# Kernel optimization log

Hardware: AMD Instinct MI355X
Metric: run time of the kernel (lower is better)

## Reference

```python
import jax, jax.numpy as jnp
import numpy as np

DIM = 512
HEADS = 8
DH = DIM // HEADS          # 64
M = DIM // 2               # 256 landmarks
PINV_ITERS = 6
KERNEL = 33                # residual_conv_kernel (lucidrains default)
SCALE = DH ** -0.5
LN_EPS = 1e-5


def setup_inputs() -> dict:
    key = jax.random.key(0)
    ks = jax.random.split(key, 6)
    b, n = 4, 4096
    x = jax.random.normal(ks[0], (b, n, DIM), jnp.float32)
    ln_w = jnp.ones((DIM,), jnp.float32)
    ln_b = jnp.zeros((DIM,), jnp.float32)
    w_qkv = jax.random.normal(ks[1], (DIM, 3 * DIM), jnp.float32) / np.float32(np.sqrt(DIM))
    w_out = jax.random.normal(ks[2], (DIM, DIM), jnp.float32) / np.float32(np.sqrt(DIM))
    b_out = jnp.zeros((DIM,), jnp.float32)
    # depthwise Conv2d(heads, heads, (33,1), groups=heads, bias=False): OIHW = (8,1,33,1)
    conv_w = jax.random.normal(ks[3], (HEADS, 1, KERNEL, 1), jnp.float32) / np.float32(np.sqrt(KERNEL))
    # admin_torch.as_module(8): residual x*omega + f(x), omega learnable scalar init sqrt(8)
    omega = jnp.asarray(np.sqrt(8.0), jnp.float32)
    return dict(x=x, ln_w=ln_w, ln_b=ln_b, w_qkv=w_qkv, w_out=w_out,
                b_out=b_out, conv_w=conv_w, omega=omega)


def _layernorm(x, w, b):
    mu = x.mean(-1, keepdims=True)
    var = x.var(-1, keepdims=True)
    return (x - mu) * jax.lax.rsqrt(var + LN_EPS) * w + b


def _moore_penrose_pinv(x, iters):
    # Newton-Schulz iteration, exactly as lucidrains nystrom-attention
    abs_x = jnp.abs(x)
    col = abs_x.sum(-1)
    row = abs_x.sum(-2)
    z = jnp.swapaxes(x, -1, -2) / (jnp.max(col) * jnp.max(row))
    I = jnp.eye(x.shape[-1], dtype=x.dtype)
    for _ in range(iters):
        xz = x @ z
        z = 0.25 * z @ (13. * I - xz @ (15. * I - xz @ (7. * I - xz)))
    return z


def reference(x, ln_w, ln_b, w_qkv, w_out, b_out, conv_w, omega):
    b, n, _ = x.shape
    nx = _layernorm(x, ln_w, ln_b)
    qkv = nx @ w_qkv                                # [b, n, 3*dim]
    q, k, v = jnp.split(qkv, 3, axis=-1)
    to_heads = lambda t: t.reshape(b, n, HEADS, DH).transpose(0, 2, 1, 3)  # bhnd
    q = to_heads(q) * SCALE
    k = to_heads(k)
    v = to_heads(v)
    l = n // M                                      # tokens per landmark group
    q_l = q.reshape(b, HEADS, M, l, DH).mean(3)     # [b,h,m,d]
    k_l = k.reshape(b, HEADS, M, l, DH).mean(3)
    sim1 = jnp.einsum('bhid,bhjd->bhij', q, k_l)    # [b,h,n,m]
    sim2 = jnp.einsum('bhid,bhjd->bhij', q_l, k_l)  # [b,h,m,m]
    sim3 = jnp.einsum('bhid,bhjd->bhij', q_l, k)    # [b,h,m,n]
    a1 = jax.nn.softmax(sim1, -1)
    a2 = jax.nn.softmax(sim2, -1)
    a3 = jax.nn.softmax(sim3, -1)
    a2_inv = _moore_penrose_pinv(a2, PINV_ITERS)
    out = (a1 @ a2_inv) @ (a3 @ v)                  # [b,h,n,d]
    # residual depthwise conv along the sequence dim of v
    res = jax.lax.conv_general_dilated(
        v, conv_w, window_strides=(1, 1),
        padding=((KERNEL // 2, KERNEL // 2), (0, 0)),
        dimension_numbers=('NCHW', 'OIHW', 'NCHW'),
        feature_group_count=HEADS)
    out = out + res
    out = out.transpose(0, 2, 1, 3).reshape(b, n, HEADS * DH)
    out = out @ w_out + b_out                       # to_out (dropout is eval no-op)
    return x * omega + out                          # admin residual
```

## Files before the change

### kernel.cpp

```cpp
#include <hip/hip_runtime.h>
#include <math.h>

#define B_    4
#define N_    4096
#define DIM_  512
#define H_    8
#define DH_   64
#define M_    256
#define LGRP  16
#define BH_   (B_*H_)
#define SCALE_ 0.125f
#define LN_EPS_ 1e-5f

#define SZ_QKVH (B_*H_*N_*DH_)
#define SZ_LM   (BH_*M_*DH_)
#define SZ_MM   (BH_*M_*M_)

typedef unsigned short ushort_t;
typedef __attribute__((ext_vector_type(8))) short bfrag8;
typedef __attribute__((ext_vector_type(4))) float fvec4;

__device__ __forceinline__ ushort_t f2b(float f) {
    unsigned u = __float_as_uint(f);
    unsigned r = (u + 0x7fffu + ((u >> 16) & 1u)) >> 16;
    return (ushort_t)r;
}
__device__ __forceinline__ float b2f(ushort_t s) {
    return __uint_as_float(((unsigned)s) << 16);
}

__device__ __forceinline__ void gload16(const ushort_t* g, ushort_t* l) {
    __builtin_amdgcn_global_load_lds(
        (const __attribute__((address_space(1))) void*)g,
        (__attribute__((address_space(3))) void*)l, 16, 0, 0);
}

__global__ __launch_bounds__(256) void ln_kernel(const float* __restrict__ x,
                                                 const float* __restrict__ w,
                                                 const float* __restrict__ bb,
                                                 ushort_t* __restrict__ nxb) {
    int row = blockIdx.x;
    int t = threadIdx.x;
    const float* xr = x + (size_t)row * DIM_;
    float v0 = xr[t], v1 = xr[t + 256];
    float s = v0 + v1, sq = v0 * v0 + v1 * v1;
    __shared__ float ls[4], lq[4];
    for (int off = 32; off > 0; off >>= 1) {
        s  += __shfl_down(s, off);
        sq += __shfl_down(sq, off);
    }
    int wid = t >> 6, lid = t & 63;
    if (lid == 0) { ls[wid] = s; lq[wid] = sq; }
    __syncthreads();
    if (t == 0) {
        float S = 0, Q = 0;
        for (int i = 0; i < 4; i++) { S += ls[i]; Q += lq[i]; }
        ls[0] = S; lq[0] = Q;
    }
    __syncthreads();
    float mean = ls[0] * (1.f / DIM_);
    float var  = lq[0] * (1.f / DIM_) - mean * mean;
    float rs = rsqrtf(var + LN_EPS_);
    ushort_t* o = nxb + (size_t)row * DIM_;
    o[t]       = f2b((v0 - mean) * rs * w[t]       + bb[t]);
    o[t + 256] = f2b((v1 - mean) * rs * w[t + 256] + bb[t + 256]);
}

__global__ __launch_bounds__(256) void tcast(const float* __restrict__ in,
                                             ushort_t* __restrict__ outT,
                                             int R, int C) {
    __shared__ float tile[32][33];
    int c0 = blockIdx.x * 32, r0 = blockIdx.y * 32;
    int t = threadIdx.x;
    #pragma unroll
    for (int u = 0; u < 4; u++) {
        int lin = t + 256 * u;
        int r = lin >> 5, c = lin & 31;
        tile[r][c] = in[(size_t)(r0 + r) * C + c0 + c];
    }
    __syncthreads();
    #pragma unroll
    for (int u = 0; u < 4; u++) {
        int lin = t + 256 * u;
        int cc = lin >> 5, rr = lin & 31;
        outT[(size_t)(c0 + cc) * R + r0 + rr] = f2b(tile[rr][cc]);
    }
}

template<int EPI>
__global__ __launch_bounds__(256) void gemm_bt128(const ushort_t* __restrict__ A,
                                                  const ushort_t* __restrict__ BT,
                                                  ushort_t* __restrict__ qb,
                                                  ushort_t* __restrict__ kb,
                                                  ushort_t* __restrict__ vb,
                                                  const float* __restrict__ x,
                                                  const float* __restrict__ bo,
                                                  const float* __restrict__ omega,
                                                  float* __restrict__ out) {
    const int K = 512;
    __shared__ __align__(16) ushort_t smem[4 * 128 * 64];
    int t = threadIdx.x;
    int lin = blockIdx.x + blockIdx.y * gridDim.x;
    int nwg = gridDim.x * gridDim.y;
    int wg  = (lin & 7) * (nwg >> 3) + (lin >> 3);
    int n0 = (wg % gridDim.x) * 128, m0 = (wg / gridDim.x) * 128;
    int w = t >> 6, lane = t & 63;
    int wr = (w >> 1) * 64, wc = (w & 1) * 64;
    int l15 = lane & 15, quad = lane >> 4, kq = quad * 8;
    int lrow = lane >> 3, lc8 = (lane & 7) * 8;
    int scol = lc8 ^ ((lrow & 7) << 3);
    int sw   = (l15 & 7) << 3;
    fvec4 acc[4][4] = {};

    auto stage = [&](int buf, int kc) {
        ushort_t* Ad = smem + buf * 16384;
        ushort_t* Bd = Ad + 8192;
        #pragma unroll
        for (int u = 0; u < 4; u++) {
            int r0 = (w << 5) + (u << 3);
            int row = r0 + lrow;
            const ushort_t* ga;
            if (EPI == 0) {
                ga = A + (size_t)(m0 + row) * K + kc + scol;
            } else {
                int grow = m0 + row; int b_ = grow >> 12, nn = grow & 4095;
                ga = A + (((size_t)(b_ * H_ + (kc >> 6)) * N_ + nn) << 6) + scol;
            }
            gload16(ga, Ad + r0 * 64);
            gload16(BT + (size_t)(n0 + row) * K + kc + scol, Bd + r0 * 64);
        }
    };

    stage(0, 0);
    __syncthreads();
    int cur = 0;
    for (int kt = 0; kt < 8; ++kt) {
        if (kt < 7) stage(cur ^ 1, (kt + 1) * 64);
        const ushort_t* As = smem + cur * 16384;
        const ushort_t* Bs = As + 8192;
        #pragma unroll
        for (int ks = 0; ks < 64; ks += 32) {
            int kcol = (ks + kq) ^ sw;
            bfrag8 a[4], b[4];
            #pragma unroll
            for (int r = 0; r < 4; r++) a[r] = *(bfrag8*)(As + (wr + r * 16 + l15) * 64 + kcol);
            #pragma unroll
            for (int c = 0; c < 4; c++) b[c] = *(bfrag8*)(Bs + (wc + c * 16 + l15) * 64 + kcol);
            #pragma unroll
            for (int r = 0; r < 4; r++)
                #pragma unroll
                for (int c = 0; c < 4; c++)
                    acc[r][c] = __builtin_amdgcn_mfma_f32_16x16x32_bf16(a[r], b[c], acc[r][c], 0, 0, 0);
        }
        __syncthreads();
        cur ^= 1;
    }

    if (EPI == 0) {
        int sec = n0 >> 9;
        float mul = (sec == 0) ? SCALE_ : 1.0f;
        ushort_t (*Ct)[132] = (ushort_t(*)[132])smem;
        #pragma unroll
        for (int r = 0; r < 4; r++) {
            #pragma unroll
            for (int reg = 0; reg < 4; reg++) {
                int lr = wr + r * 16 + quad * 4 + reg;
                #pragma unroll
                for (int c = 0; c < 4; c++) {
                    int lc = wc + c * 16 + l15;
                    Ct[lr][lc] = f2b(acc[r][c][reg] * mul);
                }
            }
        }
        __syncthreads();
        int row = t & 127, half = t >> 7;
        int grow = m0 + row; int b_ = grow >> 12, nn = grow & 4095;
        int head = ((n0 & 511) >> 6) + half;
        ushort_t* dstbuf = (sec == 0) ? qb : ((sec == 1) ? kb : vb);
        ushort_t* dp = dstbuf + (((size_t)(b_ * H_ + head) * N_ + nn) << 6);
        #pragma unroll
        for (int i = 0; i < 8; i++)
            *(uint4*)(dp + i * 8) = *(uint4*)&Ct[row][half * 64 + i * 8];
    } else {
        float om = omega[0];
        #pragma unroll
        for (int r = 0; r < 4; r++) {
            #pragma unroll
            for (int reg = 0; reg < 4; reg++) {
                int grow = m0 + wr + r * 16 + quad * 4 + reg;
                #pragma unroll
                for (int c = 0; c < 4; c++) {
                    int gcol = n0 + wc + c * 16 + l15;
                    size_t o = (size_t)grow * DIM_ + gcol;
                    out[o] = om * x[o] + bo[gcol] + acc[r][c][reg];
                }
            }
        }
    }
}

__global__ __launch_bounds__(256) void landmark_kernel(const ushort_t* __restrict__ q,
                                                       const ushort_t* __restrict__ k,
                                                       ushort_t* __restrict__ ql,
                                                       ushort_t* __restrict__ kl) {
    int idx = blockIdx.x * 256 + threadIdx.x;
    const ushort_t* src = blockIdx.y ? k : q;
    ushort_t* dst = blockIdx.y ? kl : ql;
    int d8 = (idx & 7) * 8;
    int m = (idx >> 3) & 255;
    int bh = idx >> 11;
    const ushort_t* p = src + (((size_t)bh * N_) + m * LGRP) * DH_ + d8;
    float s[8] = {};
    #pragma unroll
    for (int j = 0; j < LGRP; j++) {
        union { uint4 u4; ushort_t sv[8]; } val;
        val.u4 = *(const uint4*)(p + (size_t)j * DH_);
        #pragma unroll
        for (int e = 0; e < 8; e++) s[e] += b2f(val.sv[e]);
    }
    union { uint4 u4; ushort_t sv[8]; } o;
    #pragma unroll
    for (int e = 0; e < 8; e++) o.sv[e] = f2b(s[e] * (1.f / LGRP));
    *(uint4*)(dst + ((size_t)bh * M_ + m) * DH_ + d8) = o.u4;
}

__global__ __launch_bounds__(256) void sim2_softmax(const ushort_t* __restrict__ ql,
                                                    const ushort_t* __restrict__ kl,
                                                    float* __restrict__ a2,
                                                    ushort_t* __restrict__ a2b) {
    int i = blockIdx.x, bh = blockIdx.y, j = threadIdx.x;
    __shared__ float qrow[64];
    __shared__ float red[256];
    if (j < 64) qrow[j] = b2f(ql[((size_t)bh * M_ + i) * DH_ + j]);
    __syncthreads();
    const ushort_t* kr = kl + ((size_t)bh * M_ + j) * DH_;
    float s = 0;
    #pragma unroll
    for (int d = 0; d < 64; d++) s += qrow[d] * b2f(kr[d]);
    red[j] = s; __syncthreads();
    for (int off = 128; off > 0; off >>= 1) {
        if (j < off) red[j] = fmaxf(red[j], red[j + off]);
        __syncthreads();
    }
    float mx = red[0]; __syncthreads();
    float p = __expf(s - mx);
    red[j] = p; __syncthreads();
    for (int off = 128; off > 0; off >>= 1) {
        if (j < off) red[j] += red[j + off];
        __syncthreads();
    }
    float res = p / red[0];
    size_t o = ((size_t)bh * M_ + i) * M_ + j;
    a2[o] = res;
    a2b[o] = f2b(res);
}

__global__ void zero2(unsigned* p) { if (threadIdx.x < 2) p[threadIdx.x] = 0u; }

__global__ __launch_bounds__(256) void colpart(const float* __restrict__ a2,
                                               float* __restrict__ cs2) {
    int bh = blockIdx.x, s = blockIdx.y, t = threadIdx.x;
    const float* A = a2 + ((size_t)bh << 16) + (size_t)s * 32 * M_;
    float cs = 0.f;
    #pragma unroll
    for (int i = 0; i < 32; i++) cs += A[(size_t)i * M_ + t];
    cs2[((size_t)s * BH_ + bh) * M_ + t] = cs;
}

__global__ __launch_bounds__(256) void colmax(const float* __restrict__ cs2, unsigned* red) {
    int bh = blockIdx.x, t = threadIdx.x;
    float v = 0.f;
    #pragma unroll
    for (int s = 0; s < 8; s++) v += cs2[((size_t)s * BH_ + bh) * M_ + t];
    __shared__ float lr[256];
    lr[t] = v; __syncthreads();
    for (int off = 128; off > 0; off >>= 1) {
        if (t < off) lr[t] = fmaxf(lr[t], lr[t + off]);
        __syncthreads();
    }
    if (t == 0) atomicMax(red, __float_as_uint(lr[0]));
}

__global__ __launch_bounds__(256) void pinv_init2(const float* __restrict__ a2,
                                                  const unsigned* __restrict__ red,
                                                  ushort_t* __restrict__ zA,
                                                  ushort_t* __restrict__ zAT) {
    __shared__ float tile[32][33];
    int bt = blockIdx.z; int j0 = blockIdx.x * 32, i0 = blockIdx.y * 32;
    float invd = 1.f / __uint_as_float(red[0]);
    const float* Ab = a2 + ((size_t)bt << 16);
    size_t bo = (size_t)bt << 16;
    int t = threadIdx.x;
    #pragma unroll
    for (int u = 0; u < 4; u++) {
        int lin = t + 256 * u; int r = lin >> 5, c = lin & 31;
        float vv = Ab[(size_t)(i0 + r) * M_ + j0 + c] * invd;
        tile[r][c] = vv;
        zAT[bo + (size_t)(i0 + r) * M_ + j0 + c] = f2b(vv);
    }
    __syncthreads();
    #pragma unroll
    for (int u = 0; u < 4; u++) {
        int lin = t + 256 * u; int cc = lin >> 5, rr = lin & 31;
        zA[bo + (size_t)(j0 + cc) * M_ + i0 + rr] = f2b(tile[rr][cc]);
    }
}

__global__ __launch_bounds__(256) void gemm_pinv(const ushort_t* __restrict__ A,
                                                 const ushort_t* __restrict__ BT,
                                                 ushort_t* __restrict__ outN,
                                                 ushort_t* __restrict__ outT,
                                                 ushort_t* __restrict__ outT1,
                                                 float* __restrict__ outF,
                                                 float coefI, float scale) {
    __shared__ __align__(16) ushort_t smem[2 * 8192];
    int t = threadIdx.x;
    int lin = blockIdx.x + (blockIdx.y << 2) + (blockIdx.z << 4);
    int wg  = (lin & 7) * 64 + (lin >> 3);
    int n0 = (wg & 3) * 64, m0 = ((wg >> 2) & 3) * 64;
    int bt = wg >> 4;
    const ushort_t* Ab = A + ((size_t)bt << 16);
    const ushort_t* Bb = BT + ((size_t)bt << 16);
    int w = t >> 6, lane = t & 63;
    int wr = (w >> 1) * 32, wc = (w & 1) * 32;
    int l15 = lane & 15, quad = lane >> 4, kq = quad * 8;
    int lrow = lane >> 3, lc8 = (lane & 7) * 8;
    int scol = lc8 ^ ((lrow & 7) << 3);
    int sw   = (l15 & 7) << 3;
    fvec4 acc[2][2] = {};

    auto stage = [&](int buf, int kc) {
        ushort_t* Ad = smem + buf * 8192;
        ushort_t* Bd = Ad + 4096;
        #pragma unroll
        for (int u = 0; u < 2; u++) {
            int r0 = (w << 4) + (u << 3);
            int row = r0 + lrow;
            gload16(Ab + (size_t)(m0 + row) * M_ + kc + scol, Ad + r0 * 64);
            gload16(Bb + (size_t)(n0 + row) * M_ + kc + scol, Bd + r0 * 64);
        }
    };

    stage(0, 0);
    __syncthreads();
    int cur = 0;
    for (int kt = 0; kt < 4; ++kt) {
        if (kt < 3) stage(cur ^ 1, (kt + 1) * 64);
        const ushort_t* As = smem + cur * 8192;
        const ushort_t* Bs = As + 4096;
        #pragma unroll
        for (int ks = 0; ks < 64; ks += 32) {
            int kcol = (ks + kq) ^ sw;
            bfrag8 a[2], b[2];
            #pragma unroll
            for (int r = 0; r < 2; r++) a[r] = *(bfrag8*)(As + (wr + r * 16 + l15) * 64 + kcol);
            #pragma unroll
            for (int c = 0; c < 2; c++) b[c] = *(bfrag8*)(Bs + (wc + c * 16 + l15) * 64 + kcol);
            #pragma unroll
            for (int r = 0; r < 2; r++)
                #pragma unroll
                for (int c = 0; c < 2; c++)
                    acc[r][c] = __builtin_amdgcn_mfma_f32_16x16x32_bf16(a[r], b[c], acc[r][c], 0, 0, 0);
        }
        __syncthreads();
        cur ^= 1;
    }

    size_t bto = (size_t)bt << 16;
    if (outN || outF) {
        #pragma unroll
        for (int r = 0; r < 2; r++) {
            #pragma unroll
            for (int reg = 0; reg < 4; reg++) {
                int grow = m0 + wr + r * 16 + quad * 4 + reg;
                #pragma unroll
                for (int c = 0; c < 2; c++) {
                    int gcol = n0 + wc + c * 16 + l15;
                    float cv = scale * acc[r][c][reg] + (grow == gcol ? coefI : 0.f);
                    if (outN) outN[bto + (size_t)grow * M_ + gcol] = f2b(cv);
                    if (outF) outF[bto + (size_t)grow * M_ + gcol] = cv;
                }
            }
        }
    }
    if (outT || outT1) {
        ushort_t (*Ct)[65] = (ushort_t(*)[65])&smem[0];
        #pragma unroll
        for (int r = 0; r < 2; r++) {
            #pragma unroll
            for (int reg = 0; reg < 4; reg++) {
                int lr = wr + r * 16 + quad * 4 + reg;
                #pragma unroll
                for (int c = 0; c < 2; c++) {
                    int lc = wc + c * 16 + l15;
                    float cv = scale * acc[r][c][reg] + ((m0 + lr) == (n0 + lc) ? coefI : 0.f);
                    Ct[lr][lc] = f2b(cv);
                }
            }
        }
        __syncthreads();
        int j = t & 63, quarter = t >> 6, i0 = quarter * 16;
        #pragma unroll
        for (int vq = 0; vq < 2; vq++) {
            union { uint4 u4; ushort_t s[8]; } o1, o2;
            #pragma unroll
            for (int e = 0; e < 8; e++) {
                int il = i0 + vq * 8 + e;
                ushort_t bv = Ct[il][j];
                o1.s[e] = bv;
                o2.s[e] = f2b(((m0 + il) == (n0 + j) ? 7.f : 0.f) - b2f(bv));
            }
            size_t dst = bto + (size_t)(n0 + j) * M_ + m0 + i0 + vq * 8;
            if (outT)  *(uint4*)&outT[dst]  = o1.u4;
            if (outT1) *(uint4*)&outT1[dst] = o2.u4;
        }
    }
}

template<int NCH, int TRANSV>
__global__ __launch_bounds__(256) void flash_mfma(const ushort_t* __restrict__ Q,
                                                  const ushort_t* __restrict__ K,
                                                  const ushort_t* __restrict__ V,
                                                  ushort_t* __restrict__ Obf,
                                                  float* __restrict__ Opart,
                                                  float* __restrict__ lout,
                                                  int nq, int nk) {
    int bh = blockIdx.y;
    int nqt = nq >> 6;
    int qt = blockIdx.x % nqt;
    int ch = blockIdx.x / nqt;
    int q0 = qt * 64;
    int chunk = nk / NCH;
    int j0 = ch * chunk, j1 = j0 + chunk;

    __shared__ __align__(16) ushort_t qs[64][72];
    __shared__ __align__(16) ushort_t ks[64][72];
    __shared__ __align__(16) ushort_t vts[64][72];
    __shared__ __align__(16) ushort_t pb[64][72];

    int t = threadIdx.x;
    int w = t >> 6, lane = t & 63;
    int l15 = lane & 15, quad = lane >> 4, kq = quad * 8;
    int wrow = w * 16;

    const ushort_t* Qb = Q + ((size_t)bh * nq + q0) * DH_;
    #pragma unroll
    for (int u = 0; u < 2; u++) {
        int lin = t + 256 * u;
        int r = lin >> 3, cc = (lin & 7) * 8;
        *(uint4*)&qs[r][cc] = *(const uint4*)(Qb + r * DH_ + cc);
    }

    fvec4 Oacc[4];
    #pragma unroll
    for (int nt = 0; nt < 4; nt++)
        #pragma unroll
        for (int reg = 0; reg < 4; reg++) Oacc[nt][reg] = 0.f;
    float l_[4] = {0.f, 0.f, 0.f, 0.f};

    const ushort_t* VTbase = V + (size_t)bh * DH_ * nk;

    uint4 kreg[2], vreg[2];
    auto loadkv = [&](int j) {
        const ushort_t* Kb = K + ((size_t)bh * nk + j) * DH_;
        #pragma unroll
        for (int u = 0; u < 2; u++) {
            int lin = t + 256 * u;
            int r = lin >> 3, cc = (lin & 7) * 8;
            kreg[u] = *(const uint4*)(Kb + r * DH_ + cc);
            if (TRANSV == 0)
                vreg[u] = *(const uint4*)(VTbase + (size_t)r * nk + j + cc);
            else
                vreg[u] = *(const uint4*)(V + ((size_t)(bh * nk + j + r)) * DH_ + cc);
        }
    };
    auto writekv = [&]() {
        #pragma unroll
        for (int u = 0; u < 2; u++) {
            int lin = t + 256 * u;
            int r = lin >> 3, cc = (lin & 7) * 8;
            *(uint4*)&ks[r][cc] = kreg[u];
            if (TRANSV == 0) {
                *(uint4*)&vts[r][cc] = vreg[u];
            } else {
                union { uint4 u4; ushort_t s[8]; } vv;
                vv.u4 = vreg[u];
                #pragma unroll
                for (int m = 0; m < 8; m++) vts[cc + m][r] = vv.s[m];
            }
        }
    };

    loadkv(j0);
    for (int j = j0; j < j1; j += 64) {
        writekv();
        __syncthreads();
        if (j + 64 < j1) loadkv(j + 64);

        fvec4 S[4];
        #pragma unroll
        for (int ct = 0; ct < 4; ct++)
            #pragma unroll
            for (int reg = 0; reg < 4; reg++) S[ct][reg] = 0.f;
        bfrag8 aq0 = *(bfrag8*)&qs[wrow + l15][kq];
        bfrag8 aq1 = *(bfrag8*)&qs[wrow + l15][32 + kq];
        #pragma unroll
        for (int ct = 0; ct < 4; ct++) {
            bfrag8 b0 = *(bfrag8*)&ks[ct * 16 + l15][kq];
            bfrag8 b1 = *(bfrag8*)&ks[ct * 16 + l15][32 + kq];
            S[ct] = __builtin_amdgcn_mfma_f32_16x16x32_bf16(aq0, b0, S[ct], 0, 0, 0);
            S[ct] = __builtin_amdgcn_mfma_f32_16x16x32_bf16(aq1, b1, S[ct], 0, 0, 0);
        }

        float ps[4] = {0.f, 0.f, 0.f, 0.f};
        #pragma unroll
        for (int ct = 0; ct < 4; ct++) {
            #pragma unroll
            for (int reg = 0; reg < 4; reg++) {
                float pv = __expf(S[ct][reg]);
                ps[reg] += pv;
                pb[wrow + quad * 4 + reg][ct * 16 + l15] = f2b(pv);
            }
        }
        #pragma unroll
        for (int reg = 0; reg < 4; reg++) {
            float s = ps[reg];
            s += __shfl_xor(s, 1);
            s += __shfl_xor(s, 2);
            s += __shfl_xor(s, 4);
            s += __shfl_xor(s, 8);
            l_[reg] += s;
        }

        bfrag8 ap0 = *(bfrag8*)&pb[wrow + l15][kq];
        bfrag8 ap1 = *(bfrag8*)&pb[wrow + l15][32 + kq];
        #pragma unroll
        for (int nt = 0; nt < 4; nt++) {
            bfrag8 b0 = *(bfrag8*)&vts[nt * 16 + l15][kq];
            bfrag8 b1 = *(bfrag8*)&vts[nt * 16 + l15][32 + kq];
            Oacc[nt] = __builtin_amdgcn_mfma_f32_16x16x32_bf16(ap0, b0, Oacc[nt], 0, 0, 0);
            Oacc[nt] = __builtin_amdgcn_mfma_f32_16x16x32_bf16(ap1, b1, Oacc[nt], 0, 0, 0);
        }
        __syncthreads();
    }

    if (NCH == 1) {
        #pragma unroll
        for (int reg = 0; reg < 4; reg++) {
            float inv = 1.f / l_[reg];
            #pragma unroll
            for (int nt = 0; nt < 4; nt++)
                qs[wrow + quad * 4 + reg][nt * 16 + l15] = f2b(Oacc[nt][reg] * inv);
        }
        __syncthreads();
        ushort_t* Ob = Obf + ((size_t)bh * nq + q0) * DH_;
        #pragma unroll
        for (int u = 0; u < 2; u++) {
            int lin = t + 256 * u;
            int r = lin >> 3, i = (lin & 7) * 8;
            *(uint4*)(Ob + (size_t)r * DH_ + i) = *(uint4*)&qs[r][i];
        }
    } else {
        float (*Of)[68] = (float(*)[68])&ks[0][0];
        #pragma unroll
        for (int reg = 0; reg < 4; reg++)
            #pragma unroll
            for (int nt = 0; nt < 4; nt++)
                Of[wrow + quad * 4 + reg][nt * 16 + l15] = Oacc[nt][reg];
        size_t rows_per_ch = (size_t)BH_ * nq;
        size_t rowbase = (size_t)ch * rows_per_ch + (size_t)bh * nq + q0;
        if (l15 == 0) {
            #pragma unroll
            for (int reg = 0; reg < 4; reg++)
                lout[rowbase + wrow + quad * 4 + reg] = l_[reg];
        }
        __syncthreads();
        int orow = t >> 2, oc = (t & 3) * 16;
        float* Od = Opart + (rowbase + orow) * DH_ + oc;
        #pragma unroll
        for (int i = 0; i < 4; i++) {
            float4 v4 = make_float4(Of[orow][oc + i * 4], Of[orow][oc + i * 4 + 1],
                                    Of[orow][oc + i * 4 + 2], Of[orow][oc + i * 4 + 3]);
            *(float4*)(Od + i * 4) = v4;
        }
    }
}

__global__ __launch_bounds__(256) void flash_combine(const float* __restrict__ apart,
                                                     const float* __restrict__ lpart,
                                                     ushort_t* __restrict__ a3vb) {
    int idx = blockIdx.x * 256 + threadIdx.x;
    int d = idx & 63; int row = idx >> 6;
    const int R = BH_ * M_;
    size_t e = (size_t)row * DH_ + d;
    const size_t CH = (size_t)R * DH_;
    float l = 0.f, o = 0.f;
    #pragma unroll
    for (int s = 0; s < 4; s++) {
        l += lpart[row + (size_t)s * R];
        o += apart[e + (size_t)s * CH];
    }
    a3vb[e] = f2b(o / l);
}

__global__ __launch_bounds__(256) void flash_big(const ushort_t* __restrict__ Q,
                                                 const ushort_t* __restrict__ K,
                                                 const ushort_t* __restrict__ VT,
                                                 ushort_t* __restrict__ Obf) {
    const int nq = N_, nk = M_;
    int bh = blockIdx.y;
    int q0 = blockIdx.x * 256;
    __shared__ __align__(16) ushort_t ks[64][72];
    __shared__ __align__(16) ushort_t vts[64][72];
    __shared__ __align__(16) ushort_t pb[2][64][72];

    int t = threadIdx.x;
    int w = t >> 6, lane = t & 63;
    int l15 = lane & 15, quad = lane >> 4, kq = quad * 8;
    int wrow = w * 16;

    bfrag8 aq[4][2];
    const ushort_t* Qb = Q + ((size_t)bh * nq + q0) * DH_;
    #pragma unroll
    for (int s = 0; s < 4; s++) {
        #pragma unroll
        for (int u = 0; u < 2; u++) {
            int lin = t + 256 * u;
            int r = lin >> 3, cc = (lin & 7) * 8;
            *(uint4*)&pb[0][r][cc] = *(const uint4*)(Qb + (size_t)(s * 64 + r) * DH_ + cc);
        }
        __syncthreads();
        aq[s][0] = *(bfrag8*)&pb[0][wrow + l15][kq];
        aq[s][1] = *(bfrag8*)&pb[0][wrow + l15][32 + kq];
        __syncthreads();
    }

    fvec4 Oacc[4][4];
    #pragma unroll
    for (int s = 0; s < 4; s++)
        #pragma unroll
        for (int nt = 0; nt < 4; nt++)
            #pragma unroll
            for (int reg = 0; reg < 4; reg++) Oacc[s][nt][reg] = 0.f;
    float l_[4][4];
    #pragma unroll
    for (int s = 0; s < 4; s++)
        #pragma unroll
        for (int reg = 0; reg < 4; reg++) l_[s][reg] = 0.f;

    const ushort_t* VTb = VT + (size_t)bh * DH_ * nk;
    uint4 kreg[2], vreg[2];
    auto loadkv = [&](int j) {
        const ushort_t* Kb = K + ((size_t)bh * nk + j) * DH_;
        #pragma unroll
        for (int u = 0; u < 2; u++) {
            int lin = t + 256 * u;
            int r = lin >> 3, cc = (lin & 7) * 8;
            kreg[u] = *(const uint4*)(Kb + (size_t)r * DH_ + cc);
            vreg[u] = *(const uint4*)(VTb + (size_t)r * nk + j + cc);
        }
    };

    loadkv(0);
    for (int j = 0; j < nk; j += 64) {
        #pragma unroll
        for (int u = 0; u < 2; u++) {
            int lin = t + 256 * u;
            int r = lin >> 3, cc = (lin & 7) * 8;
            *(uint4*)&ks[r][cc] = kreg[u];
            *(uint4*)&vts[r][cc] = vreg[u];
        }
        __syncthreads();
        if (j + 64 < nk) loadkv(j + 64);

        #pragma unroll
        for (int s = 0; s < 4; s++) {
            fvec4 S[4];
            #pragma unroll
            for (int ct = 0; ct < 4; ct++)
                #pragma unroll
                for (int reg = 0; reg < 4; reg++) S[ct][reg] = 0.f;
            #pragma unroll
            for (int ct = 0; ct < 4; ct++) {
                bfrag8 b0 = *(bfrag8*)&ks[ct * 16 + l15][kq];
                bfrag8 b1 = *(bfrag8*)&ks[ct * 16 + l15][32 + kq];
                S[ct] = __builtin_amdgcn_mfma_f32_16x16x32_bf16(aq[s][0], b0, S[ct], 0, 0, 0);
                S[ct] = __builtin_amdgcn_mfma_f32_16x16x32_bf16(aq[s][1], b1, S[ct], 0, 0, 0);
            }
            float ps[4] = {0.f, 0.f, 0.f, 0.f};
            #pragma unroll
            for (int ct = 0; ct < 4; ct++) {
                #pragma unroll
                for (int reg = 0; reg < 4; reg++) {
                    float pv = __expf(S[ct][reg]);
                    ps[reg] += pv;
                    pb[s & 1][wrow + quad * 4 + reg][ct * 16 + l15] = f2b(pv);
                }
            }
            #pragma unroll
            for (int reg = 0; reg < 4; reg++) {
                float sm = ps[reg];
                sm += __shfl_xor(sm, 1);
                sm += __shfl_xor(sm, 2);
                sm += __shfl_xor(sm, 4);
                sm += __shfl_xor(sm, 8);
                l_[s][reg] += sm;
            }
            bfrag8 ap0 = *(bfrag8*)&pb[s & 1][wrow + l15][kq];
            bfrag8 ap1 = *(bfrag8*)&pb[s & 1][wrow + l15][32 + kq];
            #pragma unroll
            for (int nt = 0; nt < 4; nt++) {
                bfrag8 v0 = *(bfrag8*)&vts[nt * 16 + l15][kq];
                bfrag8 v1 = *(bfrag8*)&vts[nt * 16 + l15][32 + kq];
                Oacc[s][nt] = __builtin_amdgcn_mfma_f32_16x16x32_bf16(ap0, v0, Oacc[s][nt], 0, 0, 0);
                Oacc[s][nt] = __builtin_amdgcn_mfma_f32_16x16x32_bf16(ap1, v1, Oacc[s][nt], 0, 0, 0);
            }
        }
        __syncthreads();
    }

    ushort_t* Ob = Obf + ((size_t)bh * nq + q0) * DH_;
    #pragma unroll
    for (int s = 0; s < 4; s++) {
        #pragma unroll
        for (int reg = 0; reg < 4; reg++) {
            float inv = 1.f / l_[s][reg];
            #pragma unroll
            for (int nt = 0; nt < 4; nt++)
                pb[0][wrow + quad * 4 + reg][nt * 16 + l15] = f2b(Oacc[s][nt][reg] * inv);
        }
        __syncthreads();
        #pragma unroll
        for (int u = 0; u < 2; u++) {
            int lin = t + 256 * u;
            int r = lin >> 3, i = (lin & 7) * 8;
            *(uint4*)(Ob + (size_t)(s * 64 + r) * DH_ + i) = *(uint4*)&pb[0][r][i];
        }
        __syncthreads();
    }
}

__global__ __launch_bounds__(256) void wm_mfma(const ushort_t* __restrict__ Z,
                                               const ushort_t* __restrict__ A3V,
                                               ushort_t* __restrict__ WmT) {
    __shared__ __align__(16) ushort_t As[64][72];
    __shared__ __align__(16) ushort_t Bs[64][72];
    int bh = blockIdx.y;
    int i0 = blockIdx.x * 64;
    const ushort_t* Zb = Z + ((size_t)bh << 16);
    const ushort_t* Ab = A3V + ((size_t)bh << 14);
    int t = threadIdx.x;
    int w = t >> 6, lane = t & 63;
    int wr = (w >> 1) * 32, wc = (w & 1) * 32;
    int l15 = lane & 15, quad = lane >> 4, kq = quad * 8;
    fvec4 acc[2][2] = {};
    int rbase = t >> 3, c8 = (t & 7) * 8;

    for (int kc = 0; kc < M_; kc += 64) {
        #pragma unroll
        for (int u = 0; u < 2; u++) {
            int rr = rbase + 32 * u;
            *(float4*)&Bs[rr][c8] = *(const float4*)(Zb + (size_t)(i0 + rr) * M_ + kc + c8);
            union { uint4 u4; ushort_t s[8]; } av;
            av.u4 = *(const uint4*)(Ab + (size_t)(kc + rr) * DH_ + c8);
            #pragma unroll
            for (int m = 0; m < 8; m++) As[c8 + m][rr] = av.s[m];
        }
        __syncthreads();
        #pragma unroll
        for (int ks = 0; ks < 64; ks += 32) {
            bfrag8 a[2], b[2];
            #pragma unroll
            for (int r = 0; r < 2; r++) a[r] = *(bfrag8*)&As[wr + r * 16 + l15][ks + kq];
            #pragma unroll
            for (int c = 0; c < 2; c++) b[c] = *(bfrag8*)&Bs[wc + c * 16 + l15][ks + kq];
            #pragma unroll
            for (int r = 0; r < 2; r++)
                #pragma unroll
                for (int c = 0; c < 2; c++)
                    acc[r][c] = __builtin_amdgcn_mfma_f32_16x16x32_bf16(a[r], b[c], acc[r][c], 0, 0, 0);
        }
        __syncthreads();
    }
    #pragma unroll
    for (int r = 0; r < 2; r++) {
        #pragma unroll
        for (int reg = 0; reg < 4; reg++) {
            int drow = wr + r * 16 + quad * 4 + reg;
            ushort_t* dp = WmT + ((size_t)bh * DH_ + drow) * M_;
            #pragma unroll
            for (int c = 0; c < 2; c++)
                dp[i0 + wc + c * 16 + l15] = f2b(acc[r][c][reg]);
        }
    }
}

__global__ __launch_bounds__(256) void conv_kernel(const ushort_t* __restrict__ V,
                                                   const float* __restrict__ cw,
                                                   const ushort_t* __restrict__ ctxb,
                                                   ushort_t* __restrict__ outb) {
    int bh = blockIdx.y;
    int h = bh & 7;
    int i0 = blockIdx.x * 64;
    __shared__ float vb[96][64];
    __shared__ float wloc[33];
    int t = threadIdx.x;
    if (t < 33) wloc[t] = cw[h * 33 + t];
    #pragma unroll
    for (int u = 0; u < 3; u++) {
        int lin = t + 256 * u;
        int r = lin >> 3, cc = (lin & 7) * 8;
        int gi = i0 - 16 + r;
        union { uint4 u4; ushort_t s[8]; } val;
        if (gi >= 0 && gi < N_)
            val.u4 = *(const uint4*)(V + ((size_t)bh * N_ + gi) * DH_ + cc);
        else
            val.u4 = make_uint4(0, 0, 0, 0);
        #pragma unroll
        for (int m = 0; m < 8; m++) vb[r][cc + m] = b2f(val.s[m]);
    }
    __syncthreads();
    int d = t & 63, rb = t >> 6;
    for (int u = 0; u < 16; u++) {
        int r = rb * 16 + u;
        float s = 0.f;
        #pragma unroll
        for (int kk = 0; kk < 33; kk++) s += wloc[kk] * vb[r + kk][d];
        size_t o = ((size_t)bh * N_ + i0 + r) * DH_ + d;
        outb[o] = f2b(b2f(ctxb[o]) + s);
    }
}

extern "C" void kernel_launch(void* const* d_in, const int* in_sizes, int n_in,
                              void* d_out, int out_size, void* d_ws, size_t ws_size,
                              hipStream_t stream) {
    const float* x      = (const float*)d_in[0];
    const float* ln_w   = (const float*)d_in[1];
    const float* ln_b   = (const float*)d_in[2];
    const float* w_qkv  = (const float*)d_in[3];
    const float* w_out  = (const float*)d_in[4];
    const float* b_out  = (const float*)d_in[5];
    const float* conv_w = (const float*)d_in[6];
    const float* omega  = (const float*)d_in[7];
    float* out = (float*)d_out;

    float* fp = (float*)d_ws;
    float* a2    = fp;              fp += SZ_MM;
    float* apart = fp;              fp += SZ_QKVH / 4;
    float* lpart = fp;              fp += 4 * BH_ * M_;
    float* cs2   = fp;              fp += 8 * BH_ * M_;
    ushort_t* us = (ushort_t*)fp;
    ushort_t* wqkvT = us;           us += DIM_ * 3 * DIM_;
    ushort_t* woT   = us;           us += DIM_ * DIM_;
    ushort_t* a2b   = us;           us += SZ_MM;
    ushort_t* zA    = us;           us += SZ_MM;
    ushort_t* zAT   = us;           us += SZ_MM;
    ushort_t* zB    = us;           us += SZ_MM;
    ushort_t* zBT   = us;           us += SZ_MM;
    ushort_t* qb    = us;           us += SZ_QKVH;
    ushort_t* kb    = us;           us += SZ_QKVH;
    ushort_t* vb    = us;           us += SZ_QKVH;
    ushort_t* ctxb  = us;           us += SZ_QKVH;
    ushort_t* outhb = us;           us += SZ_QKVH;
    ushort_t* ql    = us;           us += SZ_LM;
    ushort_t* kl    = us;           us += SZ_LM;
    ushort_t* WmT   = us;           us += SZ_LM;
    ushort_t* a3vb  = us;           us += SZ_LM;
    unsigned* red   = (unsigned*)us;
    ushort_t* nxb = outhb;
    ushort_t* xz  = ctxb;
    ushort_t* t1T = xz  + SZ_MM;
    ushort_t* t2T = t1T + SZ_MM;
    ushort_t* t3T = t2T + SZ_MM;

    ln_kernel<<<B_ * N_, 256, 0, stream>>>(x, ln_w, ln_b, nxb);
    tcast<<<dim3(48, 16), 256, 0, stream>>>(w_qkv, wqkvT, DIM_, 3 * DIM_);
    tcast<<<dim3(16, 16), 256, 0, stream>>>(w_out, woT, DIM_, DIM_);
    gemm_bt128<0><<<dim3(12, 128), 256, 0, stream>>>(nxb, wqkvT, qb, kb, vb,
                                                     nullptr, nullptr, nullptr, nullptr);
    landmark_kernel<<<dim3(256, 2), 256, 0, stream>>>(qb, kb, ql, kl);
    sim2_softmax<<<dim3(M_, BH_), 256, 0, stream>>>(ql, kl, a2, a2b);
    zero2<<<1, 64, 0, stream>>>(red);
    colpart<<<dim3(BH_, 8), 256, 0, stream>>>(a2, cs2);
    colmax<<<BH_, 256, 0, stream>>>(cs2, red);
    pinv_init2<<<dim3(8, 8, 32), 256, 0, stream>>>(a2, red, zA, zAT);

    ushort_t* za = zA;  ushort_t* zaT = zAT;
    ushort_t* zb = zB;  ushort_t* zbT = zBT;
    for (int it = 0; it < 6; it++) {
        gemm_pinv<<<dim3(4, 4, BH_), 256, 0, stream>>>(a2b, zaT, xz, nullptr, t1T, nullptr, 0.f, 1.f);
        gemm_pinv<<<dim3(4, 4, BH_), 256, 0, stream>>>(xz, t1T, nullptr, t2T, nullptr, nullptr, 15.f, -1.f);
        gemm_pinv<<<dim3(4, 4, BH_), 256, 0, stream>>>(xz, t2T, nullptr, t3T, nullptr, nullptr, 13.f, -1.f);
        gemm_pinv<<<dim3(4, 4, BH_), 256, 0, stream>>>(za, t3T, zb, (it < 5) ? zbT : nullptr,
                                                       nullptr, nullptr, 0.f, 0.25f);
        ushort_t* tp;
        tp = za; za = zb; zb = tp;
        tp = zaT; zaT = zbT; zbT = tp;
    }

    flash_mfma<4, 1><<<dim3(16, BH_), 256, 0, stream>>>(ql, kb, vb, nullptr, apart, lpart, M_, N_);
    flash_combine<<<(BH_ * M_ * DH_) / 256, 256, 0, stream>>>(apart, lpart, a3vb);
    wm_mfma<<<dim3(4, BH_), 256, 0, stream>>>(za, a3vb, WmT);
    flash_big<<<dim3(N_ / 256, BH_), 256, 0, stream>>>(qb, kl, WmT, ctxb);
    conv_kernel<<<dim3(N_ / 64, BH_), 256, 0, stream>>>(vb, conv_w, ctxb, outhb);
    gemm_bt128<1><<<dim3(4, 128), 256, 0, stream>>>(outhb, woT, nullptr, nullptr, nullptr,
                                                    x, b_out, omega, out);
}
```

Baseline: 488.0 us.

## Process all 256 landmark queries per block in a3·v to reuse K/V tiles

```diff
diff --git a/kernel.cpp b/kernel.cpp
--- a/kernel.cpp
+++ b/kernel.cpp
@@ -417,166 +417,149 @@
     }
 }
 
-template<int NCH, int TRANSV>
-__global__ __launch_bounds__(256) void flash_mfma(const ushort_t* __restrict__ Q,
-                                                  const ushort_t* __restrict__ K,
-                                                  const ushort_t* __restrict__ V,
-                                                  ushort_t* __restrict__ Obf,
-                                                  float* __restrict__ Opart,
-                                                  float* __restrict__ lout,
-                                                  int nq, int nk) {
-    int bh = blockIdx.y;
-    int nqt = nq >> 6;
-    int qt = blockIdx.x % nqt;
-    int ch = blockIdx.x / nqt;
-    int q0 = qt * 64;
-    int chunk = nk / NCH;
-    int j0 = ch * chunk, j1 = j0 + chunk;
-
-    __shared__ __align__(16) ushort_t qs[64][72];
-    __shared__ __align__(16) ushort_t ks[64][72];
-    __shared__ __align__(16) ushort_t vts[64][72];
-    __shared__ __align__(16) ushort_t pb[64][72];
+__global__ __launch_bounds__(256) void flash_a3v(const ushort_t* __restrict__ Q,
+                                                 const ushort_t* __restrict__ K,
+                                                 const ushort_t* __restrict__ V,
+                                                 float* __restrict__ Opart,
+                                                 float* __restrict__ lout) {
+    const int nk = N_;
+    const int CHUNK = N_ / 8;
+    int bh = blockIdx.y, ch = blockIdx.x;
+    int j0 = ch * CHUNK, j1 = j0 + CHUNK;
+
+    __shared__ __align__(16) ushort_t smem[4 * 64 * 72];
+    ushort_t (*ks)[72]  = (ushort_t(*)[72])smem;
+    ushort_t (*vts)[72] = (ushort_t(*)[72])(smem + 64 * 72);
+    ushort_t (*pb)[64][72] = (ushort_t(*)[64][72])(smem + 2 * 64 * 72);
 
     int t = threadIdx.x;
     int w = t >> 6, lane = t & 63;
     int l15 = lane & 15, quad = lane >> 4, kq = quad * 8;
     int wrow = w * 16;
 
-    const ushort_t* Qb = Q + ((size_t)bh * nq + q0) * DH_;
-    #pragma unroll
-    for (int u = 0; u < 2; u++) {
-        int lin = t + 256 * u;
-        int r = lin >> 3, cc = (lin & 7) * 8;
-        *(uint4*)&qs[r][cc] = *(const uint4*)(Qb + r * DH_ + cc);
-    }
-
-    fvec4 Oacc[4];
-    #pragma unroll
-    for (int nt = 0; nt < 4; nt++)
-        #pragma unroll
-        for (int reg = 0; reg < 4; reg++) Oacc[nt][reg] = 0.f;
-    float l_[4] = {0.f, 0.f, 0.f, 0.f};
-
-    const ushort_t* VTbase = V + (size_t)bh * DH_ * nk;
+    bfrag8 aq[4][2];
+    const ushort_t* Qb = Q + (size_t)bh * M_ * DH_;
+    #pragma unroll
+    for (int s = 0; s < 4; s++) {
+        #pragma unroll
+        for (int u = 0; u < 2; u++) {
+            int lin = t + 256 * u;
+            int r = lin >> 3, cc = (lin & 7) * 8;
+            *(uint4*)&pb[0][r][cc] = *(const uint4*)(Qb + (size_t)(s * 64 + r) * DH_ + cc);
+        }
+        __syncthreads();
+        aq[s][0] = *(bfrag8*)&pb[0][wrow + l15][kq];
+        aq[s][1] = *(bfrag8*)&pb[0][wrow + l15][32 + kq];
+        __syncthreads();
+    }
+
+    fvec4 Oacc[4][4];
+    #pragma unroll
+    for (int s = 0; s < 4; s++)
+        #pragma unroll
+        for (int nt = 0; nt < 4; nt++)
+            #pragma unroll
+            for (int reg = 0; reg < 4; reg++) Oacc[s][nt][reg] = 0.f;
+    float l_[4][4];
+    #pragma unroll
+    for (int s = 0; s < 4; s++)
+        #pragma unroll
+        for (int reg = 0; reg < 4; reg++) l_[s][reg] = 0.f;
 
     uint4 kreg[2], vreg[2];
     auto loadkv = [&](int j) {
         const ushort_t* Kb = K + ((size_t)bh * nk + j) * DH_;
+        const ushort_t* Vb = V + ((size_t)bh * nk + j) * DH_;
         #pragma unroll
         for (int u = 0; u < 2; u++) {
             int lin = t + 256 * u;
             int r = lin >> 3, cc = (lin & 7) * 8;
-            kreg[u] = *(const uint4*)(Kb + r * DH_ + cc);
-            if (TRANSV == 0)
-                vreg[u] = *(const uint4*)(VTbase + (size_t)r * nk + j + cc);
-            else
-                vreg[u] = *(const uint4*)(V + ((size_t)(bh * nk + j + r)) * DH_ + cc);
+            kreg[u] = *(const uint4*)(Kb + (size_t)r * DH_ + cc);
+            vreg[u] = *(const uint4*)(Vb + (size_t)r * DH_ + cc);
         }
     };
-    auto writekv = [&]() {
+
+    loadkv(j0);
+    for (int j = j0; j < j1; j += 64) {
         #pragma unroll
         for (int u = 0; u < 2; u++) {
             int lin = t + 256 * u;
             int r = lin >> 3, cc = (lin & 7) * 8;
             *(uint4*)&ks[r][cc] = kreg[u];
-            if (TRANSV == 0) {
-                *(uint4*)&vts[r][cc] = vreg[u];
-            } else {
-                union { uint4 u4; ushort_t s[8]; } vv;
-                vv.u4 = vreg[u];
-                #pragma unroll
-                for (int m = 0; m < 8; m++) vts[cc + m][r] = vv.s[m];
-            }
-        }
-    };
-
-    loadkv(j0);
-    for (int j = j0; j < j1; j += 64) {
-        writekv();
+            union { uint4 u4; ushort_t s[8]; } vv;
+            vv.u4 = vreg[u];
+            #pragma unroll
+            for (int m = 0; m < 8; m++) vts[cc + m][r] = vv.s[m];
+        }
         __syncthreads();
         if (j + 64 < j1) loadkv(j + 64);
 
-        fvec4 S[4];
-        #pragma unroll
-        for (int ct = 0; ct < 4; ct++)
-            #pragma unroll
-            for (int reg = 0; reg < 4; reg++) S[ct][reg] = 0.f;
-        bfrag8 aq0 = *(bfrag8*)&qs[wrow + l15][kq];
-        bfrag8 aq1 = *(bfrag8*)&qs[wrow + l15][32 + kq];
-        #pragma unroll
-        for (int ct = 0; ct < 4; ct++) {
-            bfrag8 b0 = *(bfrag8*)&ks[ct * 16 + l15][kq];
-            bfrag8 b1 = *(bfrag8*)&ks[ct * 16 + l15][32 + kq];
-            S[ct] = __builtin_amdgcn_mfma_f32_16x16x32_bf16(aq0, b0, S[ct], 0, 0, 0);
-            S[ct] = __builtin_amdgcn_mfma_f32_16x16x32_bf16(aq1, b1, S[ct], 0, 0, 0);
-        }
-
-        float ps[4] = {0.f, 0.f, 0.f, 0.f};
-        #pragma unroll
-        for (int ct = 0; ct < 4; ct++) {
+        #pragma unroll
+        for (int s = 0; s < 4; s++) {
+            fvec4 S[4];
+            #pragma unroll
+            for (int ct = 0; ct < 4; ct++)
+                #pragma unroll
+                for (int reg = 0; reg < 4; reg++) S[ct][reg] = 0.f;
+            #pragma unroll
+            for (int ct = 0; ct < 4; ct++) {
+                bfrag8 b0 = *(bfrag8*)&ks[ct * 16 + l15][kq];
+                bfrag8 b1 = *(bfrag8*)&ks[ct * 16 + l15][32 + kq];
+                S[ct] = __builtin_amdgcn_mfma_f32_16x16x32_bf16(aq[s][0], b0, S[ct], 0, 0, 0);
+                S[ct] = __builtin_amdgcn_mfma_f32_16x16x32_bf16(aq[s][1], b1, S[ct], 0, 0, 0);
+            }
+            float ps[4] = {0.f, 0.f, 0.f, 0.f};
+            #pragma unroll
+            for (int ct = 0; ct < 4; ct++) {
+                #pragma unroll
+                for (int reg = 0; reg < 4; reg++) {
+                    float pv = __expf(S[ct][reg]);
+                    ps[reg] += pv;
+                    pb[s & 1][wrow + quad * 4 + reg][ct * 16 + l15] = f2b(pv);
+                }
+            }
             #pragma unroll
             for (int reg = 0; reg < 4; reg++) {
-                float pv = __expf(S[ct][reg]);
-                ps[reg] += pv;
-                pb[wrow + quad * 4 + reg][ct * 16 + l15] = f2b(pv);
-            }
-        }
+                float sm = ps[reg];
+                sm += __shfl_xor(sm, 1);
+                sm += __shfl_xor(sm, 2);
+                sm += __shfl_xor(sm, 4);
+                sm += __shfl_xor(sm, 8);
+                l_[s][reg] += sm;
+            }
+            bfrag8 ap0 = *(bfrag8*)&pb[s & 1][wrow + l15][kq];
+            bfrag8 ap1 = *(bfrag8*)&pb[s & 1][wrow + l15][32 + kq];
+            #pragma unroll
+            for (int nt = 0; nt < 4; nt++) {
+                bfrag8 v0 = *(bfrag8*)&vts[nt * 16 + l15][kq];
+                bfrag8 v1 = *(bfrag8*)&vts[nt * 16 + l15][32 + kq];
+                Oacc[s][nt] = __builtin_amdgcn_mfma_f32_16x16x32_bf16(ap0, v0, Oacc[s][nt], 0, 0, 0);
+                Oacc[s][nt] = __builtin_amdgcn_mfma_f32_16x16x32_bf16(ap1, v1, Oacc[s][nt], 0, 0, 0);
+            }
+        }
+        __syncthreads();
+    }
+
+    float (*Of)[68] = (float(*)[68])smem;
+    const size_t R = (size_t)BH_ * M_;
+    size_t rowbase = (size_t)ch * R + (size_t)bh * M_;
+    #pragma unroll
+    for (int s = 0; s < 4; s++) {
+        __syncthreads();
         #pragma unroll
         for (int reg = 0; reg < 4; reg++) {
-            float s = ps[reg];
-            s += __shfl_xor(s, 1);
-            s += __shfl_xor(s, 2);
-            s += __shfl_xor(s, 4);
-            s += __shfl_xor(s, 8);
-            l_[reg] += s;
-        }
-
-        bfrag8 ap0 = *(bfrag8*)&pb[wrow + l15][kq];
-        bfrag8 ap1 = *(bfrag8*)&pb[wrow + l15][32 + kq];
-        #pragma unroll
-        for (int nt = 0; nt < 4; nt++) {
-            bfrag8 b0 = *(bfrag8*)&vts[nt * 16 + l15][kq];
-            bfrag8 b1 = *(bfrag8*)&vts[nt * 16 + l15][32 + kq];
-            Oacc[nt] = __builtin_amdgcn_mfma_f32_16x16x32_bf16(ap0, b0, Oacc[nt], 0, 0, 0);
-            Oacc[nt] = __builtin_amdgcn_mfma_f32_16x16x32_bf16(ap1, b1, Oacc[nt], 0, 0, 0);
-        }
-        __syncthreads();
-    }
-
-    if (NCH == 1) {
-        #pragma unroll
-        for (int reg = 0; reg < 4; reg++) {
-            float inv = 1.f / l_[reg];
             #pragma unroll
             for (int nt = 0; nt < 4; nt++)
-                qs[wrow + quad * 4 + reg][nt * 16 + l15] = f2b(Oacc[nt][reg] * inv);
-        }
-        __syncthreads();
-        ushort_t* Ob = Obf + ((size_t)bh * nq + q0) * DH_;
-        #pragma unroll
-        for (int u = 0; u < 2; u++) {
-            int lin = t + 256 * u;
-            int r = lin >> 3, i = (lin & 7) * 8;
-            *(uint4*)(Ob + (size_t)r * DH_ + i) = *(uint4*)&qs[r][i];
-        }
-    } else {
-        float (*Of)[68] = (float(*)[68])&ks[0][0];
-        #pragma unroll
-        for (int reg = 0; reg < 4; reg++)
-            #pragma unroll
-            for (int nt = 0; nt < 4; nt++)
-                Of[wrow + quad * 4 + reg][nt * 16 + l15] = Oacc[nt][reg];
-        size_t rows_per_ch = (size_t)BH_ * nq;
-        size_t rowbase = (size_t)ch * rows_per_ch + (size_t)bh * nq + q0;
+                Of[wrow + quad * 4 + reg][nt * 16 + l15] = Oacc[s][nt][reg];
+        }
         if (l15 == 0) {
             #pragma unroll
             for (int reg = 0; reg < 4; reg++)
-                lout[rowbase + wrow + quad * 4 + reg] = l_[reg];
+                lout[rowbase + s * 64 + wrow + quad * 4 + reg] = l_[s][reg];
         }
         __syncthreads();
         int orow = t >> 2, oc = (t & 3) * 16;
-        float* Od = Opart + (rowbase + orow) * DH_ + oc;
+        float* Od = Opart + (rowbase + s * 64 + orow) * DH_ + oc;
         #pragma unroll
         for (int i = 0; i < 4; i++) {
             float4 v4 = make_float4(Of[orow][oc + i * 4], Of[orow][oc + i * 4 + 1],
@@ -596,7 +579,7 @@
     const size_t CH = (size_t)R * DH_;
     float l = 0.f, o = 0.f;
     #pragma unroll
-    for (int s = 0; s < 4; s++) {
+    for (int s = 0; s < 8; s++) {
         l += lpart[row + (size_t)s * R];
         o += apart[e + (size_t)s * CH];
     }
@@ -846,8 +829,8 @@
 
     float* fp = (float*)d_ws;
     float* a2    = fp;              fp += SZ_MM;
-    float* apart = fp;              fp += SZ_QKVH / 4;
-    float* lpart = fp;              fp += 4 * BH_ * M_;
+    float* apart = fp;              fp += SZ_QKVH / 2;
+    float* lpart = fp;              fp += 8 * BH_ * M_;
     float* cs2   = fp;              fp += 8 * BH_ * M_;
     ushort_t* us = (ushort_t*)fp;
     ushort_t* wqkvT = us;           us += DIM_ * 3 * DIM_;
@@ -898,7 +881,7 @@
         tp = zaT; zaT = zbT; zbT = tp;
     }
 
-    flash_mfma<4, 1><<<dim3(16, BH_), 256, 0, stream>>>(ql, kb, vb, nullptr, apart, lpart, M_, N_);
+    flash_a3v<<<dim3(8, BH_), 256, 0, stream>>>(ql, kb, vb, apart, lpart);
     flash_combine<<<(BH_ * M_ * DH_) / 256, 256, 0, stream>>>(apart, lpart, a3vb);
     wm_mfma<<<dim3(4, BH_), 256, 0, stream>>>(za, a3vb, WmT);
     flash_big<<<dim3(N_ / 256, BH_), 256, 0, stream>>>(qb, kl, WmT, ctxb);
```

After: 497.4 us. No clear change (+1.9%).
